# Performance work log

Hardware: AMD Instinct MI355X
Metric: run time of the kernel (lower is better)

The kernel has to match this reference:

```python
import jax, jax.numpy as jnp
import numpy as np

B, S, E, H, M, K, FF = 4, 256, 1024, 16, 65536, 32, 4096
HD = E // H
LN_EPS = 1e-5


def _ln(x, g, b):
    mu = jnp.mean(x, axis=-1, keepdims=True)
    var = jnp.var(x, axis=-1, keepdims=True)
    return (x - mu) * jax.lax.rsqrt(var + LN_EPS) * g + b


def _mha(q, k, v, wq, bq, wk, bk, wv, bv, wo, bo):
    Bq, Sq, _ = q.shape
    Sk = k.shape[1]
    Q = (q @ wq + bq).reshape(Bq, Sq, H, HD)
    Kh = (k @ wk + bk).reshape(Bq, Sk, H, HD)
    V = (v @ wv + bv).reshape(Bq, Sk, H, HD)
    scores = jnp.einsum('bqhd,bkhd->bhqk', Q, Kh) / np.float32(np.sqrt(HD))
    attn = jax.nn.softmax(scores, axis=-1)
    out = jnp.einsum('bhqk,bkhd->bqhd', attn, V).reshape(Bq, Sq, E)
    return out @ wo + bo


def setup_inputs() -> dict:
    key = jax.random.key(0)
    ks = iter(jax.random.split(key, 16))
    d = {
        'x': jax.random.normal(next(ks), (B, S, E), jnp.float32),
        'mem_keys': jax.random.normal(next(ks), (M, E), jnp.float32),
        'mem_vals': jax.random.normal(next(ks), (M, E), jnp.float32),
    }
    for p in ('sa', 'ma'):
        for w in ('wq', 'wk', 'wv', 'wo'):
            d[f'{p}_{w}'] = 0.02 * jax.random.normal(next(ks), (E, E), jnp.float32)
        for bname in ('bq', 'bk', 'bv', 'bo'):
            d[f'{p}_{bname}'] = jnp.zeros((E,), jnp.float32)
    for ln in ('ln1', 'ln2', 'ln3'):
        d[f'{ln}_g'] = jnp.ones((E,), jnp.float32)
        d[f'{ln}_b'] = jnp.zeros((E,), jnp.float32)
    d['fc1_w'] = 0.02 * jax.random.normal(next(ks), (E, FF), jnp.float32)
    d['fc1_b'] = jnp.zeros((FF,), jnp.float32)
    d['fc2_w'] = 0.02 * jax.random.normal(next(ks), (FF, E), jnp.float32)
    d['fc2_b'] = jnp.zeros((E,), jnp.float32)
    return d


def reference(x, mem_keys, mem_vals,
              sa_wq, sa_bq, sa_wk, sa_bk, sa_wv, sa_bv, sa_wo, sa_bo,
              ma_wq, ma_bq, ma_wk, ma_bk, ma_wv, ma_bv, ma_wo, ma_bo,
              ln1_g, ln1_b, ln2_g, ln2_b, ln3_g, ln3_b,
              fc1_w, fc1_b, fc2_w, fc2_b):
    # self-attention block (eval mode -> dropout is identity)
    a = _mha(x, x, x, sa_wq, sa_bq, sa_wk, sa_bk, sa_wv, sa_bv, sa_wo, sa_bo)
    x1 = _ln(x + a, ln1_g, ln1_b)
    # kNN retrieval: cosine sim -> top-k -> gather values
    qn = x1 / jnp.maximum(jnp.linalg.norm(x1, axis=-1, keepdims=True), 1e-12)
    mkn = mem_keys / jnp.maximum(jnp.linalg.norm(mem_keys, axis=-1, keepdims=True), 1e-12)
    sims = jnp.einsum('bse,me->bsm', qn, mkn)              # (B,S,M)
    _, idx = jax.lax.top_k(sims, K)                        # (B,S,K)
    retrieved = mem_vals[idx]                              # (B,S,K,E)
    rflat = retrieved.reshape(B, S * K, E)
    # memory cross-attention over retrieved values
    m = _mha(x1, rflat, rflat, ma_wq, ma_bq, ma_wk, ma_bk, ma_wv, ma_bv, ma_wo, ma_bo)
    x2 = _ln(x1 + m, ln2_g, ln2_b)
    # FFN (exact GELU, as torch default)
    h = jax.nn.gelu(x2 @ fc1_w + fc1_b, approximate=False)
    y = h @ fc2_w + fc2_b
    return _ln(x2 + y, ln3_g, ln3_b)
```

## Files before the change

kernel.cpp:

```cpp
#include <hip/hip_runtime.h>
#include <hip/hip_bf16.h>
#include <math.h>

#define DEVFN __device__ __forceinline__

typedef __attribute__((ext_vector_type(8))) short bf16x8;
typedef __attribute__((ext_vector_type(8))) unsigned short u16x8;
typedef __attribute__((ext_vector_type(4))) unsigned short u16x4;
typedef __attribute__((ext_vector_type(4))) float f32x4;

static constexpr int Bn = 4, Sn = 256, En = 1024, Hn = 16;
static constexpr int Mn = 65536, Kt = 32, FFn = 4096;
static constexpr int NT = Bn * Sn;

DEVFN unsigned short f2b(float f) {
  unsigned int u = __float_as_uint(f);
  unsigned int r = (u + 0x7FFFu + ((u >> 16) & 1u)) >> 16;
  return (unsigned short)r;
}
DEVFN float b2f(unsigned short u) { return __uint_as_float((unsigned)u << 16); }

DEVFN unsigned okey16(unsigned short u) {
  return (unsigned)(u ^ ((u >> 15) ? 0xFFFFu : 0x8000u)) & 0xFFFFu;
}

typedef const __attribute__((address_space(1))) void* as1cv_t;
typedef __attribute__((address_space(3))) void* as3v_t;
DEVFN void gload16(const void* g, void* l) {
  __builtin_amdgcn_global_load_lds((as1cv_t)g, (as3v_t)l, 16, 0, 0);
}
#define MEMFENCE asm volatile("" ::: "memory")

struct P8 { const float* s[8]; };

__global__ __launch_bounds__(256) void k_transpose8(
    P8 ps, unsigned short* __restrict__ outbase) {
  const float* in = ps.s[blockIdx.z];
  unsigned short* out = outbase + (size_t)blockIdx.z * En * En;
  __shared__ float tile[64][65];
  int tx = threadIdx.x & 63, ty = threadIdx.x >> 6;
  int c0 = blockIdx.x * 64, r0 = blockIdx.y * 64;
  #pragma unroll
  for (int i = 0; i < 16; i++) {
    int r = ty + i * 4;
    tile[tx][r] = in[(size_t)(r0 + r) * En + (c0 + tx)];
  }
  __syncthreads();
  #pragma unroll
  for (int i = 0; i < 16; i++) {
    int c = ty + i * 4;
    out[(size_t)(c0 + c) * En + (r0 + tx)] = f2b(tile[c][tx]);
  }
}

__global__ __launch_bounds__(256) void k_transpose_bf16(
    const float* __restrict__ in, unsigned short* __restrict__ out, int R, int C) {
  __shared__ float tile[64][65];
  int tx = threadIdx.x & 63, ty = threadIdx.x >> 6;
  int c0 = blockIdx.x * 64, r0 = blockIdx.y * 64;
  #pragma unroll
  for (int i = 0; i < 16; i++) {
    int r = ty + i * 4;
    tile[tx][r] = in[(size_t)(r0 + r) * C + (c0 + tx)];
  }
  __syncthreads();
  #pragma unroll
  for (int i = 0; i < 16; i++) {
    int c = ty + i * 4;
    out[(size_t)(c0 + c) * R + (r0 + tx)] = f2b(tile[c][tx]);
  }
}

__global__ __launch_bounds__(256) void k_cvt_bf16(
    const float* __restrict__ in, unsigned short* __restrict__ out, int n4) {
  int i = blockIdx.x * 256 + threadIdx.x;
  if (i >= n4) return;
  float4 v = ((const float4*)in)[i];
  uint2 o;
  o.x = (unsigned int)f2b(v.x) | ((unsigned int)f2b(v.y) << 16);
  o.y = (unsigned int)f2b(v.z) | ((unsigned int)f2b(v.w) << 16);
  ((uint2*)out)[i] = o;
}

__global__ __launch_bounds__(256) void k_gathercvt(
    const float* __restrict__ mv, const int* __restrict__ idx,
    unsigned short* __restrict__ out) {
  int r = blockIdx.x;
  int src = idx[r];
  float4 v = ((const float4*)(mv + (size_t)src * En))[threadIdx.x];
  uint2 o;
  o.x = (unsigned int)f2b(v.x) | ((unsigned int)f2b(v.y) << 16);
  o.y = (unsigned int)f2b(v.z) | ((unsigned int)f2b(v.w) << 16);
  ((uint2*)(out + (size_t)r * En))[threadIdx.x] = o;
}

__global__ __launch_bounds__(256) void k_concat3(
    const float* __restrict__ a, const float* __restrict__ b,
    const float* __restrict__ c, float* __restrict__ o) {
  int i = blockIdx.x * 256 + threadIdx.x;
  float v = (i < 1024) ? a[i] : (i < 2048) ? b[i - 1024] : c[i - 2048];
  o[i] = v;
}

__global__ __launch_bounds__(256) void k_normcvt(
    const float* __restrict__ mk, unsigned short* __restrict__ out) {
  int m = blockIdx.x, t = threadIdx.x;
  float4 v = ((const float4*)(mk + (size_t)m * En))[t];
  float ss = v.x*v.x + v.y*v.y + v.z*v.z + v.w*v.w;
  #pragma unroll
  for (int d = 32; d; d >>= 1) ss += __shfl_down(ss, d);
  __shared__ float red[4];
  int lane = t & 63, w = t >> 6;
  if (lane == 0) red[w] = ss;
  __syncthreads();
  float rs = 1.0f / fmaxf(sqrtf(red[0] + red[1] + red[2] + red[3]), 1e-12f);
  uint2 o;
  o.x = (unsigned int)f2b(v.x * rs) | ((unsigned int)f2b(v.y * rs) << 16);
  o.y = (unsigned int)f2b(v.z * rs) | ((unsigned int)f2b(v.w * rs) << 16);
  ((uint2*)(out + (size_t)m * En))[t] = o;
}

__global__ __launch_bounds__(256) void k_layernorm(
    const float* __restrict__ in, const float* __restrict__ g, const float* __restrict__ bb,
    float* __restrict__ outf, unsigned short* __restrict__ outb) {
  int n = blockIdx.x, t = threadIdx.x;
  float4 v = ((const float4*)(in + (size_t)n * En))[t];
  float s  = v.x + v.y + v.z + v.w;
  float s2 = v.x*v.x + v.y*v.y + v.z*v.z + v.w*v.w;
  #pragma unroll
  for (int d = 32; d; d >>= 1) { s += __shfl_down(s, d); s2 += __shfl_down(s2, d); }
  __shared__ float rs[4], rq[4];
  int lane = t & 63, w = t >> 6;
  if (lane == 0) { rs[w] = s; rq[w] = s2; }
  __syncthreads();
  float mean = (rs[0]+rs[1]+rs[2]+rs[3]) * (1.0f/En);
  float var  = (rq[0]+rq[1]+rq[2]+rq[3]) * (1.0f/En) - mean*mean;
  float rstd = rsqrtf(var + 1e-5f);
  float4 gg = ((const float4*)g)[t];
  float4 bv = ((const float4*)bb)[t];
  float o0 = (v.x-mean)*rstd*gg.x + bv.x;
  float o1 = (v.y-mean)*rstd*gg.y + bv.y;
  float o2 = (v.z-mean)*rstd*gg.z + bv.z;
  float o3 = (v.w-mean)*rstd*gg.w + bv.w;
  if (outf) { float4 ov = {o0,o1,o2,o3}; ((float4*)(outf + (size_t)n*En))[t] = ov; }
  if (outb) {
    uint2 o;
    o.x = (unsigned int)f2b(o0) | ((unsigned int)f2b(o1) << 16);
    o.y = (unsigned int)f2b(o2) | ((unsigned int)f2b(o3) << 16);
    ((uint2*)(outb + (size_t)n*En))[t] = o;
  }
}

__global__ __launch_bounds__(256) void k_layernorm4(
    const float* __restrict__ pp, const float* __restrict__ pbias,
    const float* __restrict__ resid,
    const float* __restrict__ g, const float* __restrict__ bb,
    float* __restrict__ outf, unsigned short* __restrict__ outb) {
  int n = blockIdx.x, t = threadIdx.x;
  const size_t PS = (size_t)NT * En / 4;
  size_t i = (size_t)n * 256 + t;
  float4 p0 = ((const float4*)pp)[i];
  float4 p1 = ((const float4*)pp)[i + PS];
  float4 p2 = ((const float4*)pp)[i + 2 * PS];
  float4 p3 = ((const float4*)pp)[i + 3 * PS];
  float4 rv = ((const float4*)(resid + (size_t)n * En))[t];
  float4 bi = ((const float4*)pbias)[t];
  float4 v;
  v.x = (p0.x + p1.x) + (p2.x + p3.x) + bi.x + rv.x;
  v.y = (p0.y + p1.y) + (p2.y + p3.y) + bi.y + rv.y;
  v.z = (p0.z + p1.z) + (p2.z + p3.z) + bi.z + rv.z;
  v.w = (p0.w + p1.w) + (p2.w + p3.w) + bi.w + rv.w;
  float s  = v.x + v.y + v.z + v.w;
  float s2 = v.x*v.x + v.y*v.y + v.z*v.z + v.w*v.w;
  #pragma unroll
  for (int d = 32; d; d >>= 1) { s += __shfl_down(s, d); s2 += __shfl_down(s2, d); }
  __shared__ float rs[4], rq[4];
  int lane = t & 63, w = t >> 6;
  if (lane == 0) { rs[w] = s; rq[w] = s2; }
  __syncthreads();
  float mean = (rs[0]+rs[1]+rs[2]+rs[3]) * (1.0f/En);
  float var  = (rq[0]+rq[1]+rq[2]+rq[3]) * (1.0f/En) - mean*mean;
  float rstd = rsqrtf(var + 1e-5f);
  float4 gg = ((const float4*)g)[t];
  float4 bv = ((const float4*)bb)[t];
  float o0 = (v.x-mean)*rstd*gg.x + bv.x;
  float o1 = (v.y-mean)*rstd*gg.y + bv.y;
  float o2 = (v.z-mean)*rstd*gg.z + bv.z;
  float o3 = (v.w-mean)*rstd*gg.w + bv.w;
  if (outf) { float4 ov = {o0,o1,o2,o3}; ((float4*)(outf + (size_t)n*En))[t] = ov; }
  if (outb) {
    uint2 o;
    o.x = (unsigned int)f2b(o0) | ((unsigned int)f2b(o1) << 16);
    o.y = (unsigned int)f2b(o2) | ((unsigned int)f2b(o3) << 16);
    ((uint2*)(outb + (size_t)n*En))[t] = o;
  }
}

template<int EPI, bool AGATHER, int NOUT, int LSWZ>
__global__ __launch_bounds__(512) void k_gemm256(
    const unsigned short* __restrict__ Ab, const unsigned short* __restrict__ Bb,
    const int* __restrict__ gidx, const float* __restrict__ bias,
    float* __restrict__ Cf, unsigned short* __restrict__ cb0, unsigned short* __restrict__ cb1,
    int Ndim, int Kdim, int nRT, int nCT) {
  extern __shared__ unsigned short lds[];
  const int t = threadIdx.x, lane = t & 63, w = t >> 6;
  const int wr = w >> 2, wc = w & 3, l15 = lane & 15, l4 = lane >> 4;
  const int lr2 = lane >> 2;
  const int cg  = (lane & 3) ^ (((lane >> 5) & 1) << 1);

  const int nwg = nRT * nCT;
  int lb = ((int)blockIdx.x % 8) * (nwg >> 3) + ((int)blockIdx.x >> 3);
  int rowT, colT;
  if (LSWZ == 0) { rowT = lb % nRT; colT = lb / nRT; }
  else           { colT = lb % nCT; rowT = lb / nCT; }
  const int row0 = rowT * 256, col0 = colT * 256;

  auto pa = [&](int h) -> unsigned short* { return lds + h * 16384; };
  auto pb = [&](int h) -> unsigned short* { return lds + h * 16384 + 8192; };

  const unsigned short *aSrc0, *aSrc1;
  if constexpr (AGATHER) {
    aSrc0 = Ab + (size_t)gidx[row0 + w * 32 + lr2] * Kdim + cg * 8;
    aSrc1 = Ab + (size_t)gidx[row0 + w * 32 + 16 + lr2] * Kdim + cg * 8;
  } else {
    aSrc0 = Ab + (size_t)(row0 + w * 32 + lr2) * Kdim + cg * 8;
    aSrc1 = aSrc0 + (size_t)16 * Kdim;
  }
  const unsigned short* bSrc0 = Bb + (size_t)(col0 + w * 32 + lr2) * Kdim + cg * 8;
  const unsigned short* bSrc1 = bSrc0 + (size_t)16 * Kdim;

  f32x4 acc[8][4];
  #pragma unroll
  for (int i = 0; i < 8; i++)
    #pragma unroll
    for (int j = 0; j < 4; j++) acc[i][j] = (f32x4){0.f, 0.f, 0.f, 0.f};

  const int NH = Kdim >> 5;
  #pragma unroll
  for (int h = 0; h < 3; ++h) {
    const int ko = h * 32;
    gload16(aSrc0 + ko, pa(h) + w*32*32);
    gload16(aSrc1 + ko, pa(h) + (w*32+16)*32);
    gload16(bSrc0 + ko, pb(h) + w*32*32);
    gload16(bSrc1 + ko, pb(h) + (w*32+16)*32);
  }
  asm volatile("s_waitcnt vmcnt(8)" ::: "memory");
  __builtin_amdgcn_s_barrier();
  MEMFENCE;

  for (int hs = 0; hs < NH; ++hs) {
    const int cur = hs & 3;
    const unsigned short* Ap = pa(cur);
    const unsigned short* Bp = pb(cur);
    const int h3 = (hs + 3) & 3, ko3 = (hs + 3) * 32;
    const bool pf = (hs + 3) < NH;
    bf16x8 bfr[4], af[4];

    #pragma unroll
    for (int ni = 0; ni < 4; ni++) {
      int row = wc * 64 + ni * 16 + l15;
      int c8 = l4 ^ (((row >> 3) & 1) << 1);
      bfr[ni] = *(const bf16x8*)&Bp[row * 32 + c8 * 8];
    }
    #pragma unroll
    for (int m = 0; m < 4; m++) {
      int row = wr * 128 + m * 16 + l15;
      int c8 = l4 ^ (((row >> 3) & 1) << 1);
      af[m] = *(const bf16x8*)&Ap[row * 32 + c8 * 8];
    }
    if (pf) {
      gload16(aSrc0 + ko3, pa(h3) + w*32*32);
      gload16(aSrc1 + ko3, pa(h3) + (w*32+16)*32);
    }
    __builtin_amdgcn_s_setprio(1);
    #pragma unroll
    for (int m = 0; m < 4; m++)
      #pragma unroll
      for (int ni = 0; ni < 4; ni++)
        acc[m][ni] = __builtin_amdgcn_mfma_f32_16x16x32_bf16(af[m], bfr[ni], acc[m][ni], 0, 0, 0);
    __builtin_amdgcn_s_setprio(0);

    #pragma unroll
    for (int m = 0; m < 4; m++) {
      int row = wr * 128 + (4 + m) * 16 + l15;
      int c8 = l4 ^ (((row >> 3) & 1) << 1);
      af[m] = *(const bf16x8*)&Ap[row * 32 + c8 * 8];
    }
    if (pf) {
      gload16(bSrc0 + ko3, pb(h3) + w*32*32);
      gload16(bSrc1 + ko3, pb(h3) + (w*32+16)*32);
    }
    __builtin_amdgcn_s_setprio(1);
    #pragma unroll
    for (int m = 0; m < 4; m++)
      #pragma unroll
      for (int ni = 0; ni < 4; ni++)
        acc[4 + m][ni] = __builtin_amdgcn_mfma_f32_16x16x32_bf16(af[m], bfr[ni], acc[4 + m][ni], 0, 0, 0);
    __builtin_amdgcn_s_setprio(0);

    if (hs + 1 < NH) {
      const int rem = NH - 2 - hs;
      if (rem >= 2)      asm volatile("s_waitcnt vmcnt(8)" ::: "memory");
      else if (rem == 1) asm volatile("s_waitcnt vmcnt(4)" ::: "memory");
      else               asm volatile("s_waitcnt vmcnt(0)" ::: "memory");
      __builtin_amdgcn_s_barrier();
      MEMFENCE;
    }
  }

  #pragma unroll
  for (int m = 0; m < 8; m++) {
    #pragma unroll
    for (int ni = 0; ni < 4; ni++) {
      int col  = col0 + wc * 64 + ni * 16 + l15;
      int rowb = row0 + wr * 128 + m * 16 + l4 * 4;
      if constexpr (EPI == 6) {
        if (col < 1024) {
          #pragma unroll
          for (int r = 0; r < 4; r++)
            cb0[(size_t)(rowb + r) * 1024 + col] = f2b(acc[m][ni][r] + bias[col]);
        } else {
          int c = col - 1024;
          int bi = rowb >> 13, k0 = rowb & 8191;
          u16x4 o;
          #pragma unroll
          for (int r = 0; r < 4; r++) o[r] = f2b(acc[m][ni][r] + bias[col]);
          *(u16x4*)&cb1[((size_t)bi * 1024 + c) * 8192 + k0] = o;
        }
      } else {
        #pragma unroll
        for (int r = 0; r < 4; r++) {
          float v = acc[m][ni][r];
          if constexpr (EPI == 4) {
            Cf[(size_t)(rowb + r) * Ndim + col] = v;
          } else if constexpr (EPI == 5) {
            cb0[(size_t)(rowb + r) * Ndim + col] = f2b(v);
          } else {
            unsigned short* cb = (col >> 10) ? cb1 : cb0;
            cb[(size_t)(rowb + r) * 1024 + (col & 1023)] = f2b(v + bias[col]);
          }
        }
      }
    }
  }
}

template<int EPI, bool AGATHER, bool SWAPG, int NOUT, bool QSC, int SK>
__global__ __launch_bounds__(256) void k_gemm(
    const unsigned short* __restrict__ Ab, const unsigned short* __restrict__ Bb,
    const int* __restrict__ gidx,
    const float* __restrict__ bias, const float* __restrict__ resid,
    float* __restrict__ Cf, unsigned short* __restrict__ cb0,
    unsigned short* __restrict__ cb1, unsigned short* __restrict__ cb2,
    int Ndim, int Kdim) {
  __shared__ unsigned short As[128][32];
  __shared__ unsigned short Bs[128][32];
  const int t = threadIdx.x, lane = t & 63, w = t >> 6;
  const int wr = w >> 1, wc = w & 1, l15 = lane & 15, l4 = lane >> 4;
  const int row0 = (SWAPG ? blockIdx.x : blockIdx.y) * 128;
  const int col0 = (SWAPG ? blockIdx.y : blockIdx.x) * 128;
  const int c8  = (lane & 3) * 8;
  const int r16 = lane >> 2;
  const int rA0 = w * 32 + r16, rA1 = rA0 + 16;
  const int koff = (SK > 1) ? (int)blockIdx.z * (Kdim / SK) : 0;
  const int kend = (SK > 1) ? koff + Kdim / SK : Kdim;

  size_t raA0, raA1, raB0, raB1;
  if constexpr (AGATHER) {
    raA0 = (size_t)gidx[row0 + rA0] * Kdim;
    raA1 = (size_t)gidx[row0 + rA1] * Kdim;
  } else {
    raA0 = (size_t)(row0 + rA0) * Kdim;
    raA1 = (size_t)(row0 + rA1) * Kdim;
  }
  raB0 = (size_t)(col0 + rA0) * Kdim;
  raB1 = (size_t)(col0 + rA1) * Kdim;

  f32x4 acc[4][4];
  #pragma unroll
  for (int i = 0; i < 4; i++)
    #pragma unroll
    for (int j = 0; j < 4; j++) acc[i][j] = (f32x4){0.f,0.f,0.f,0.f};

  for (int kt0 = koff; kt0 < kend; kt0 += 32) {
    __syncthreads();
    gload16(Ab + raA0 + kt0 + c8, &As[w * 32][0]);
    gload16(Ab + raA1 + kt0 + c8, &As[w * 32 + 16][0]);
    gload16(Bb + raB0 + kt0 + c8, &Bs[w * 32][0]);
    gload16(Bb + raB1 + kt0 + c8, &Bs[w * 32 + 16][0]);
    __syncthreads();
    bf16x8 af[4], bfr[4];
    #pragma unroll
    for (int mi = 0; mi < 4; mi++) af[mi]  = *(const bf16x8*)&As[wr*64 + mi*16 + l15][l4*8];
    #pragma unroll
    for (int ni = 0; ni < 4; ni++) bfr[ni] = *(const bf16x8*)&Bs[wc*64 + ni*16 + l15][l4*8];
    #pragma unroll
    for (int mi = 0; mi < 4; mi++)
      #pragma unroll
      for (int ni = 0; ni < 4; ni++)
        acc[mi][ni] = __builtin_amdgcn_mfma_f32_16x16x32_bf16(af[mi], bfr[ni], acc[mi][ni], 0, 0, 0);
  }

  unsigned short* cbase = cb0;
  int colsub = 0;
  float qsc = 1.0f;
  if constexpr (NOUT > 1) {
    int which = col0 >> 10;
    cbase = (which == 0) ? cb0 : (which == 1) ? cb1 : cb2;
    colsub = col0 & 1023;
    if (QSC && which == 0) qsc = 0.125f;
  } else if constexpr (QSC) {
    qsc = 0.125f;
  }
  float* Cfp = Cf;
  if constexpr (EPI == 7) Cfp = Cf + (size_t)blockIdx.z * NT * En;

  #pragma unroll
  for (int mi = 0; mi < 4; mi++) {
    #pragma unroll
    for (int ni = 0; ni < 4; ni++) {
      int col  = col0 + wc*64 + ni*16 + l15;
      int rowb = row0 + wr*64 + mi*16 + l4*4;
      #pragma unroll
      for (int r = 0; r < 4; r++) {
        float v = acc[mi][ni][r];
        size_t off = (size_t)(rowb + r) * Ndim + col;
        if constexpr (EPI == 0) {
          if constexpr (NOUT > 1) {
            int c2 = colsub + wc*64 + ni*16 + l15;
            cbase[(size_t)(rowb + r) * 1024 + c2] = f2b((v + bias[col]) * qsc);
          } else {
            cb0[off] = f2b((v + bias[col]) * qsc);
          }
        } else if constexpr (EPI == 1) {
          Cf[off] = v + bias[col] + resid[off];
        } else if constexpr (EPI == 2) {
          float u = v + bias[col];
          u = 0.5f * u * (1.0f + erff(u * 0.70710678118654752f));
          cb0[off] = f2b(u);
        } else if constexpr (EPI == 7) {
          Cfp[off] = v;
        } else {
          Cf[off] = v;
        }
      }
    }
  }
}

__global__ __launch_bounds__(256) void k_attn_sa(
    const unsigned short* __restrict__ Qp, const unsigned short* __restrict__ Kp,
    const unsigned short* __restrict__ Vp, unsigned short* __restrict__ Op, int Lk) {
  __shared__ unsigned short Ks[64][72];
  __shared__ unsigned short Vt[64][72];
  __shared__ float Ps[4][16][68];
  const int b = blockIdx.z;
  const int h = blockIdx.y, q0 = blockIdx.x * 64;
  const int t = threadIdx.x, lane = t & 63, w = t >> 6;
  const int l15 = lane & 15, l4 = lane >> 4;

  const int qrow = q0 + w * 16 + l15;
  const unsigned short* qptr = Qp + (size_t)(b * Sn + qrow) * En + h * 64 + l4 * 8;
  bf16x8 qf0 = *(const bf16x8*)qptr;
  bf16x8 qf1 = *(const bf16x8*)(qptr + 32);

  f32x4 oacc[4];
  #pragma unroll
  for (int i = 0; i < 4; i++) oacc[i] = (f32x4){0.f,0.f,0.f,0.f};
  float m_[4] = {-INFINITY, -INFINITY, -INFINITY, -INFINITY};
  float l_[4] = {0.f, 0.f, 0.f, 0.f};

  const int nkt = Lk / 64;
  for (int kt = 0; kt < nkt; ++kt) {
    __syncthreads();
    #pragma unroll
    for (int i = 0; i < 2; i++) {
      int ld = t + i * 256;
      int kr = ld >> 3, d8 = (ld & 7) * 8;
      size_t base = (size_t)(b * Lk + kt * 64 + kr) * En + h * 64 + d8;
      *(uint4*)&Ks[kr][d8] = *(const uint4*)(Kp + base);
      bf16x8 vv = *(const bf16x8*)(Vp + base);
      int colswz = kr ^ ((t & 7) << 3);
      #pragma unroll
      for (int j = 0; j < 8; j++) Vt[d8 + j][colswz] = ((unsigned short*)&vv)[j];
    }
    __syncthreads();

    f32x4 s[4];
    #pragma unroll
    for (int ni = 0; ni < 4; ni++) {
      s[ni] = (f32x4){0.f,0.f,0.f,0.f};
      bf16x8 kb0 = *(const bf16x8*)&Ks[ni*16 + l15][l4*8];
      bf16x8 kb1 = *(const bf16x8*)&Ks[ni*16 + l15][l4*8 + 32];
      s[ni] = __builtin_amdgcn_mfma_f32_16x16x32_bf16(qf0, kb0, s[ni], 0, 0, 0);
      s[ni] = __builtin_amdgcn_mfma_f32_16x16x32_bf16(qf1, kb1, s[ni], 0, 0, 0);
    }

    #pragma unroll
    for (int r = 0; r < 4; r++) {
      float mx = fmaxf(fmaxf(s[0][r], s[1][r]), fmaxf(s[2][r], s[3][r]));
      #pragma unroll
      for (int d2 = 1; d2 < 16; d2 <<= 1) mx = fmaxf(mx, __shfl_xor(mx, d2));
      float m = m_[r];
      if (mx > m + 8.f) {
        float alpha = __expf(m - mx);
        l_[r] *= alpha;
        #pragma unroll
        for (int nd = 0; nd < 4; nd++) oacc[nd][r] *= alpha;
        m = mx; m_[r] = mx;
      }
      float p0 = __expf(s[0][r] - m), p1 = __expf(s[1][r] - m);
      float p2 = __expf(s[2][r] - m), p3 = __expf(s[3][r] - m);
      s[0][r] = p0; s[1][r] = p1; s[2][r] = p2; s[3][r] = p3;
      l_[r] += (p0 + p1) + (p2 + p3);
    }

    #pragma unroll
    for (int ni = 0; ni < 4; ni++)
      #pragma unroll
      for (int r = 0; r < 4; r++)
        Ps[w][l4*4 + r][ni*16 + l15] = s[ni][r];
    asm volatile("s_waitcnt lgkmcnt(0)" ::: "memory");

    #pragma unroll
    for (int half = 0; half < 2; half++) {
      float4 pv0 = *(const float4*)&Ps[w][l15][half*32 + l4*8];
      float4 pv1 = *(const float4*)&Ps[w][l15][half*32 + l4*8 + 4];
      bf16x8 pa;
      pa[0]=(short)f2b(pv0.x); pa[1]=(short)f2b(pv0.y); pa[2]=(short)f2b(pv0.z); pa[3]=(short)f2b(pv0.w);
      pa[4]=(short)f2b(pv1.x); pa[5]=(short)f2b(pv1.y); pa[6]=(short)f2b(pv1.z); pa[7]=(short)f2b(pv1.w);
      #pragma unroll
      for (int nd = 0; nd < 4; nd++) {
        int dd = nd*16 + l15;
        bf16x8 vb = *(const bf16x8*)&Vt[dd][(half*32 + l4*8) ^ (((dd >> 3) & 7) << 3)];
        oacc[nd] = __builtin_amdgcn_mfma_f32_16x16x32_bf16(pa, vb, oacc[nd], 0, 0, 0);
      }
    }
  }

  #pragma unroll
  for (int r = 0; r < 4; r++) {
    float lv = l_[r];
    #pragma unroll
    for (int d2 = 1; d2 < 16; d2 <<= 1) lv += __shfl_xor(lv, d2);
    l_[r] = lv;
  }
  #pragma unroll
  for (int nd = 0; nd < 4; nd++)
    #pragma unroll
    for (int r = 0; r < 4; r++) {
      int q = q0 + w*16 + l4*4 + r;
      Op[(size_t)(b * Sn + q) * En + h * 64 + nd*16 + l15] = f2b(oacc[nd][r] / l_[r]);
    }
}

__global__ __launch_bounds__(256, 2) void k_attn_ma(
    const unsigned short* __restrict__ Qp, const unsigned short* __restrict__ Kp,
    const unsigned short* __restrict__ Vp,
    unsigned short* __restrict__ PO, float* __restrict__ PM, float* __restrict__ PL) {
  constexpr int Lk = Sn * Kt;
  constexpr int NTI = 8;
  __shared__ unsigned short Ks[2][64 * 64];
  __shared__ unsigned short Vt[2][64 * 64];
  __shared__ float Ps[4][16][68];
  const int sp = blockIdx.x, h = blockIdx.y, b = blockIdx.z;
  const int t = threadIdx.x, lane = t & 63, w = t >> 6;
  const int l15 = lane & 15, l4 = lane >> 4;
  const int l8 = lane >> 3, l7 = lane & 7;
  const int kswz = (l7 ^ l8) * 8;
  const int rbase = w * 16;

  bf16x8 qf[4][2];
  #pragma unroll
  for (int qt = 0; qt < 4; qt++) {
    const unsigned short* qptr = Qp + (size_t)(b * Sn + w * 64 + qt * 16 + l15) * En + h * 64 + l4 * 8;
    qf[qt][0] = *(const bf16x8*)qptr;
    qf[qt][1] = *(const bf16x8*)(qptr + 32);
  }

  f32x4 oacc[4][4];
  #pragma unroll
  for (int i = 0; i < 4; i++)
    #pragma unroll
    for (int j = 0; j < 4; j++) oacc[i][j] = (f32x4){0.f,0.f,0.f,0.f};
  float m_[4][4], l_[4][4];
  #pragma unroll
  for (int i = 0; i < 4; i++)
    #pragma unroll
    for (int j = 0; j < 4; j++) { m_[i][j] = -INFINITY; l_[i][j] = 0.f; }

  const int kt0 = sp * NTI;
  auto stage = [&](int kt, int buf) {
    #pragma unroll
    for (int i = 0; i < 2; i++) {
      int row = rbase + i * 8 + l8;
      gload16(Kp + (size_t)(b * Lk + kt * 64 + row) * En + h * 64 + kswz,
              &Ks[buf][(rbase + i * 8) * 64]);
      gload16(Vp + ((size_t)b * 1024 + h * 64 + row) * (size_t)Lk + kt * 64 + kswz,
              &Vt[buf][(rbase + i * 8) * 64]);
    }
  };

  stage(kt0, 0);
  stage(kt0 + 1, 1);
  asm volatile("s_waitcnt vmcnt(4)" ::: "memory");
  __builtin_amdgcn_s_barrier();
  MEMFENCE;

  for (int j = 0; j < NTI; ++j) {
    const int cur = j & 1;
    #pragma unroll
    for (int qt = 0; qt < 4; qt++) {
      f32x4 s[4];
      #pragma unroll
      for (int ni = 0; ni < 4; ni++) {
        s[ni] = (f32x4){0.f,0.f,0.f,0.f};
        int rowK = ni * 16 + l15, sw = (rowK & 7) * 8;
        bf16x8 kb0 = *(const bf16x8*)&Ks[cur][rowK * 64 + ((l4 * 8) ^ sw)];
        bf16x8 kb1 = *(const bf16x8*)&Ks[cur][rowK * 64 + ((l4 * 8 + 32) ^ sw)];
        s[ni] = __builtin_amdgcn_mfma_f32_16x16x32_bf16(qf[qt][0], kb0, s[ni], 0, 0, 0);
        s[ni] = __builtin_amdgcn_mfma_f32_16x16x32_bf16(qf[qt][1], kb1, s[ni], 0, 0, 0);
      }
      #pragma unroll
      for (int r = 0; r < 4; r++) {
        float mx = fmaxf(fmaxf(s[0][r], s[1][r]), fmaxf(s[2][r], s[3][r]));
        #pragma unroll
        for (int d2 = 1; d2 < 16; d2 <<= 1) mx = fmaxf(mx, __shfl_xor(mx, d2));
        float m = m_[qt][r];
        if (mx > m + 8.f) {
          float alpha = __expf(m - mx);
          l_[qt][r] *= alpha;
          #pragma unroll
          for (int nd = 0; nd < 4; nd++) oacc[qt][nd][r] *= alpha;
          m = mx; m_[qt][r] = mx;
        }
        float p0 = __expf(s[0][r] - m), p1 = __expf(s[1][r] - m);
        float p2 = __expf(s[2][r] - m), p3 = __expf(s[3][r] - m);
        s[0][r] = p0; s[1][r] = p1; s[2][r] = p2; s[3][r] = p3;
        l_[qt][r] += (p0 + p1) + (p2 + p3);
      }
      #pragma unroll
      for (int ni = 0; ni < 4; ni++)
        #pragma unroll
        for (int r = 0; r < 4; r++)
          Ps[w][l4*4 + r][ni*16 + l15] = s[ni][r];
      asm volatile("s_waitcnt lgkmcnt(0)" ::: "memory");
      #pragma unroll
      for (int half = 0; half < 2; half++) {
        float4 pv0 = *(const float4*)&Ps[w][l15][half*32 + l4*8];
        float4 pv1 = *(const float4*)&Ps[w][l15][half*32 + l4*8 + 4];
        bf16x8 pa;
        pa[0]=(short)f2b(pv0.x); pa[1]=(short)f2b(pv0.y); pa[2]=(short)f2b(pv0.z); pa[3]=(short)f2b(pv0.w);
        pa[4]=(short)f2b(pv1.x); pa[5]=(short)f2b(pv1.y); pa[6]=(short)f2b(pv1.z); pa[7]=(short)f2b(pv1.w);
        #pragma unroll
        for (int nd = 0; nd < 4; nd++) {
          int dd = nd*16 + l15;
          bf16x8 vb = *(const bf16x8*)&Vt[cur][dd * 64 + ((half*32 + l4*8) ^ ((dd & 7) * 8))];
          oacc[qt][nd] = __builtin_amdgcn_mfma_f32_16x16x32_bf16(pa, vb, oacc[qt][nd], 0, 0, 0);
        }
      }
    }
    MEMFENCE; __builtin_amdgcn_s_barrier(); MEMFENCE;
    if (j + 2 < NTI) stage(kt0 + j + 2, cur);
    if (j + 1 < NTI) {
      if (j + 2 < NTI) asm volatile("s_waitcnt vmcnt(4)" ::: "memory");
      else             asm volatile("s_waitcnt vmcnt(0)" ::: "memory");
      __builtin_amdgcn_s_barrier();
      MEMFENCE;
    }
  }

  #pragma unroll
  for (int qt = 0; qt < 4; qt++)
    #pragma unroll
    for (int r = 0; r < 4; r++) {
      float lv = l_[qt][r];
      #pragma unroll
      for (int d2 = 1; d2 < 16; d2 <<= 1) lv += __shfl_xor(lv, d2);
      l_[qt][r] = lv;
    }

  const int slot = (b * Hn + h) * 16 + sp;
  #pragma unroll
  for (int qt = 0; qt < 4; qt++)
    #pragma unroll
    for (int nd = 0; nd < 4; nd++)
      #pragma unroll
      for (int r = 0; r < 4; r++)
        PO[(size_t)slot * 16384 + (w*64 + qt*16 + l4*4 + r) * 64 + nd*16 + l15] = f2b(oacc[qt][nd][r]);
  if (l15 == 0) {
    #pragma unroll
    for (int qt = 0; qt < 4; qt++)
      #pragma unroll
      for (int r = 0; r < 4; r++) {
        PM[slot * 256 + w*64 + qt*16 + l4*4 + r] = m_[qt][r];
        PL[slot * 256 + w*64 + qt*16 + l4*4 + r] = l_[qt][r];
      }
  }
}

__global__ __launch_bounds__(256) void k_attn_comb16(
    const unsigned short* __restrict__ PO, const float* __restrict__ PM,
    const float* __restrict__ PL, unsigned short* __restrict__ Op) {
  const int W = blockIdx.x * 4 + (threadIdx.x >> 6);
  const int lane = threadIdx.x & 63;
  const int bh = W >> 8, q = W & 255;
  const int slotBase = bh * 16;
  float ms[16];
  float M = -INFINITY;
  #pragma unroll
  for (int s = 0; s < 16; s++) { ms[s] = PM[(slotBase + s) * 256 + q]; M = fmaxf(M, ms[s]); }
  float L = 0.f, acc = 0.f;
  #pragma unroll
  for (int s = 0; s < 16; s++) {
    float wgt = __expf(ms[s] - M);
    L += PL[(slotBase + s) * 256 + q] * wgt;
    acc += wgt * b2f(PO[(size_t)(slotBase + s) * 16384 + q * 64 + lane]);
  }
  const int b = bh >> 4, h = bh & 15;
  Op[(size_t)(b * Sn + q) * En + h * 64 + lane] = f2b(acc / L);
}

DEVFN unsigned blk_exscan16(unsigned part, volatile unsigned* wsum, int lane, int wid) {
  unsigned v = part;
  #pragma unroll
  for (int d = 1; d < 64; d <<= 1) { unsigned o = __shfl_up(v, d); if (lane >= d) v += o; }
  if (lane == 63) wsum[wid] = v;
  __syncthreads();
  unsigned woff = 0;
  for (int i = 0; i < wid; i++) woff += wsum[i];
  unsigned r = woff + v - part;
  __syncthreads();
  return r;
}

DEVFN void find_thr16(const unsigned* hist, int NB, unsigned need,
                      int t, int lane, int wid, volatile unsigned* wsum,
                      volatile int* s_thr, volatile unsigned* s_above) {
  int per = NB >> 10;
  int lo = NB - per * (t + 1);
  unsigned part = 0;
  for (int j = 0; j < per; j++) part += hist[lo + j];
  unsigned ex = blk_exscan16(part, wsum, lane, wid);
  if (ex < need && ex + part >= need) {
    unsigned c = ex;
    for (int j = per - 1; j >= 0; j--) {
      unsigned h = hist[lo + j];
      if (c + h >= need) { *s_thr = lo + j; *s_above = c; break; }
      c += h;
    }
  }
  __syncthreads();
}

__global__ __launch_bounds__(1024) void k_topk16(
    const unsigned short* __restrict__ simsb, int* __restrict__ oidx) {
  const int n = blockIdx.x, t = threadIdx.x;
  const int lane = t & 63, wid = t >> 6;
  const u16x8* row8 = (const u16x8*)(simsb + (size_t)n * Mn);
  constexpr unsigned CAP = 2048;
  __shared__ unsigned hist[2048];
  __shared__ unsigned wsum[16];
  __shared__ int s_thr;
  __shared__ unsigned s_above;
  __shared__ unsigned h2[32];
  __shared__ unsigned s_cnt, s_na;
  __shared__ unsigned short ckey[CAP];
  __shared__ unsigned cidx[CAP];
  __shared__ int slist[32];
  __shared__ unsigned sL, sneedEq, scntEq, s_imin;

  for (int i = t; i < 2048; i += 1024) hist[i] = 0;
  if (t < 32) h2[t] = 0;
  if (t == 0) { s_cnt = 0; s_na = 0; }
  __syncthreads();

  {
    u16x8 v = row8[3584 + t];
    #pragma unroll
    for (int j = 0; j < 8; j++) atomicAdd(&hist[okey16(v[j]) >> 5], 1u);
  }
  __syncthreads();
  find_thr16(hist, 2048, 32, t, lane, wid, wsum, &s_thr, &s_above);
  const unsigned base = ((unsigned)s_thr) << 5;

  #pragma unroll
  for (int p = 0; p < 8; p++) {
    u16x8 v = row8[p * 1024 + t];
    unsigned i0 = (unsigned)(p * 1024 + t) * 8;
    #pragma unroll
    for (int j = 0; j < 8; j++) {
      unsigned k = okey16(v[j]);
      if (k >= base) {
        unsigned slot = atomicAdd(&s_cnt, 1u);
        if (slot < CAP) { ckey[slot] = (unsigned short)k; cidx[slot] = i0 + j; }
      }
    }
  }
// ... 117 lines not shown
    unsigned cnt = 0;
    for (int p = 0; p < 8; p++) {
      u16x8 v = row8[p * 1024 + t];
      unsigned i0 = (unsigned)(p * 1024 + t) * 8;
      #pragma unroll
      for (int j = 0; j < 8; j++) {
        unsigned k = okey16(v[j]);
        cnt += (k > L || (k == L && i0 + j <= istar));
      }
    }
    unsigned pos = blk_exscan16(cnt, wsum, lane, wid);
    for (int p = 0; p < 8; p++) {
      u16x8 v = row8[p * 1024 + t];
      unsigned i0 = (unsigned)(p * 1024 + t) * 8;
      #pragma unroll
      for (int j = 0; j < 8; j++) {
        unsigned k = okey16(v[j]);
        if (k > L || (k == L && i0 + j <= istar)) oidx[n * Kt + pos++] = (int)(i0 + j);
      }
    }
  }
}

extern "C" void kernel_launch(void* const* d_in, const int* in_sizes, int n_in,
                              void* d_out, int out_size, void* d_ws, size_t ws_size,
                              hipStream_t stream) {
  (void)in_sizes; (void)n_in; (void)out_size;
  const float* x      = (const float*)d_in[0];
  const float* mem_k  = (const float*)d_in[1];
  const float* mem_v  = (const float*)d_in[2];
  const float* sa_w[4] = {(const float*)d_in[3], (const float*)d_in[4], (const float*)d_in[5], (const float*)d_in[6]};
  const float* sa_b[4] = {(const float*)d_in[7], (const float*)d_in[8], (const float*)d_in[9], (const float*)d_in[10]};
  const float* ma_w[4] = {(const float*)d_in[11], (const float*)d_in[12], (const float*)d_in[13], (const float*)d_in[14]};
  const float* ma_b[4] = {(const float*)d_in[15], (const float*)d_in[16], (const float*)d_in[17], (const float*)d_in[18]};
  const float* ln_g[3] = {(const float*)d_in[19], (const float*)d_in[21], (const float*)d_in[23]};
  const float* ln_b[3] = {(const float*)d_in[20], (const float*)d_in[22], (const float*)d_in[24]};
  const float* fc1_w = (const float*)d_in[25];
  const float* fc1_b = (const float*)d_in[26];
  const float* fc2_w = (const float*)d_in[27];
  const float* fc2_b = (const float*)d_in[28];
  float* out = (float*)d_out;

  char* ws = (char*)d_ws;
  size_t off = 0;
  auto alloc = [&](size_t bytes) -> char* {
    char* p = ws + off;
    off = (off + bytes + 255) & ~(size_t)255;
    return p;
  };

  unsigned short* wt[8];
  for (int i = 0; i < 8; i++) wt[i] = (unsigned short*)alloc((size_t)En * En * 2);
  unsigned short* fc1t  = (unsigned short*)alloc((size_t)FFn * En * 2);
  unsigned short* fc2t  = (unsigned short*)alloc((size_t)En * FFn * 2);
  unsigned short* xb    = (unsigned short*)alloc((size_t)NT * En * 2);
  unsigned short* Qb    = (unsigned short*)alloc((size_t)NT * En * 2);
  unsigned short* Kb    = (unsigned short*)alloc((size_t)NT * En * 2);
  unsigned short* Vb    = (unsigned short*)alloc((size_t)NT * En * 2);
  unsigned short* at1b  = (unsigned short*)alloc((size_t)NT * En * 2);
  float*          x1f   = (float*)alloc((size_t)NT * En * 4);
  unsigned short* x1b   = (unsigned short*)alloc((size_t)NT * En * 2);
  char*           simsRaw = alloc((size_t)NT * Mn * 4);
  int*            idx   = (int*)alloc((size_t)NT * Kt * 4);
  unsigned short* K2b   = (unsigned short*)alloc((size_t)NT * Kt * En * 2);
  unsigned short* V2b   = (unsigned short*)alloc((size_t)NT * Kt * En * 2);
  unsigned short* Q2b   = (unsigned short*)alloc((size_t)NT * En * 2);
  unsigned short* at2b  = (unsigned short*)alloc((size_t)NT * En * 2);
  float*          x2f   = (float*)alloc((size_t)NT * En * 4);
  unsigned short* x2b   = (unsigned short*)alloc((size_t)NT * En * 2);
  unsigned short* hb    = (unsigned short*)alloc((size_t)NT * FFn * 2);
  float*          pp    = (float*)alloc((size_t)4 * NT * En * 4);
  float*          bcat_sa = (float*)alloc(3072 * 4);
  float*          bcat_ma = (float*)alloc(2048 * 4);

  if (off > ws_size) return;

  unsigned short* simsb = (unsigned short*)simsRaw;
  unsigned short* mkb = (unsigned short*)K2b;
  unsigned short* Ab2 = (unsigned short*)(simsRaw + (size_t)128 * 1024 * 1024);
  unsigned short* PO  = (unsigned short*)(simsRaw + (size_t)192 * 1024 * 1024);
  float* PM = (float*)(simsRaw + (size_t)224 * 1024 * 1024);
  float* PL = (float*)(simsRaw + (size_t)225 * 1024 * 1024);

  (void)hipFuncSetAttribute((const void*)&k_gemm256<5,false,1,0>,
                            hipFuncAttributeMaxDynamicSharedMemorySize, 131072);
  (void)hipFuncSetAttribute((const void*)&k_gemm256<6,false,2,1>,
                            hipFuncAttributeMaxDynamicSharedMemorySize, 131072);

  P8 p8;
  for (int i = 0; i < 4; i++) { p8.s[i] = sa_w[i]; p8.s[4 + i] = ma_w[i]; }
  k_transpose8<<<dim3(16, 16, 8), 256, 0, stream>>>(p8, wt[0]);
  k_transpose_bf16<<<dim3(64, 16), 256, 0, stream>>>(fc1_w, fc1t, En, FFn);
  k_transpose_bf16<<<dim3(16, 64), 256, 0, stream>>>(fc2_w, fc2t, FFn, En);
  k_concat3<<<dim3(12), 256, 0, stream>>>(sa_b[0], sa_b[1], sa_b[2], bcat_sa);
  k_concat3<<<dim3(8),  256, 0, stream>>>(ma_b[1], ma_b[2], ma_b[2], bcat_ma);

  k_cvt_bf16<<<dim3(NT * En / 4 / 256), 256, 0, stream>>>(x, xb, NT * En / 4);
  k_normcvt<<<dim3(Mn), 256, 0, stream>>>(mem_k, mkb);

  const dim3 g1(En / 128, NT / 128);
  const dim3 g1s(En / 128, NT / 128, 4);

  k_gemm<0,false,false,3,true,1><<<dim3(24, 8), 256, 0, stream>>>(xb, wt[0], nullptr, bcat_sa, nullptr, nullptr, Qb, Kb, Vb, 3072, En);
  k_attn_sa<<<dim3(Sn / 64, Hn, Bn), 256, 0, stream>>>(Qb, Kb, Vb, at1b, Sn);
  k_gemm<7,false,false,1,false,4><<<g1s, 256, 0, stream>>>(at1b, wt[3], nullptr, nullptr, nullptr, pp, nullptr, nullptr, nullptr, En, En);
  k_layernorm4<<<NT, 256, 0, stream>>>(pp, sa_b[3], x, ln_g[0], ln_b[0], x1f, x1b);

  k_gemm256<5,false,1,0><<<dim3(1024), 512, 131072, stream>>>(
      x1b, mkb, nullptr, nullptr, nullptr, simsb, nullptr, Mn, En, NT / 256, Mn / 256);
  k_topk16<<<NT, 1024, 0, stream>>>(simsb, idx);

  k_gathercvt<<<dim3(NT * Kt), 256, 0, stream>>>(mem_v, idx, Ab2);
  k_gemm256<6,false,2,1><<<dim3(1024), 512, 131072, stream>>>(
      Ab2, wt[5], nullptr, bcat_ma, nullptr, K2b, V2b, 2048, En, NT * Kt / 256, 2048 / 256);
  k_gemm<0,false,false,1,true,1><<<g1, 256, 0, stream>>>(x1b, wt[4], nullptr, ma_b[0], nullptr, nullptr, Q2b, nullptr, nullptr, En, En);
  k_attn_ma<<<dim3(16, Hn, Bn), 256, 0, stream>>>(Q2b, K2b, V2b, PO, PM, PL);
  k_attn_comb16<<<dim3(Bn * Hn * Sn / 4), 256, 0, stream>>>(PO, PM, PL, at2b);
  k_gemm<7,false,false,1,false,4><<<g1s, 256, 0, stream>>>(at2b, wt[7], nullptr, nullptr, nullptr, pp, nullptr, nullptr, nullptr, En, En);
  k_layernorm4<<<NT, 256, 0, stream>>>(pp, ma_b[3], x1f, ln_g[1], ln_b[1], x2f, x2b);

  k_gemm<2,false,false,1,false,1><<<dim3(FFn / 128, NT / 128), 256, 0, stream>>>(x2b, fc1t, nullptr, fc1_b, nullptr, nullptr, hb, nullptr, nullptr, FFn, En);
  k_gemm<7,false,false,1,false,4><<<g1s, 256, 0, stream>>>(hb, fc2t, nullptr, nullptr, nullptr, pp, nullptr, nullptr, nullptr, En, FFn);
  k_layernorm4<<<NT, 256, 0, stream>>>(pp, fc2_b, x2f, ln_g[2], ln_b[2], out, nullptr);
}
```

Measured before the change: 791.1 us.

## Triple-buffer k_gemm K-loop with async LDS loads and fold log2e into Q scale

The 128x128 k_gemm loses its two-barrier single-buffer loop. It now uses a 3-stage LDS ring filled by global_load_lds with XOR-swizzled columns, waits on vmcnt so loads overlap the MFMAs, and raises wave priority around the MFMA block. The Q scale is changed from 1/sqrt(d) to 1/sqrt(d)*log2(e) so the attention softmax kernels can use exp2f instead of __expf. Unused gather, residual-epilogue and layernorm paths are removed. LDS use per block triples, which may lower occupancy.

```diff
diff --git a/kernel.cpp b/kernel.cpp
--- a/kernel.cpp
+++ b/kernel.cpp
@@ -12,6 +12,7 @@
 static constexpr int Bn = 4, Sn = 256, En = 1024, Hn = 16;
 static constexpr int Mn = 65536, Kt = 32, FFn = 4096;
 static constexpr int NT = Bn * Sn;
+static constexpr float QS = 0.18033688011112042f;
 
 DEVFN unsigned short f2b(float f) {
   unsigned int u = __float_as_uint(f);
@@ -118,37 +119,6 @@
   o.x = (unsigned int)f2b(v.x * rs) | ((unsigned int)f2b(v.y * rs) << 16);
   o.y = (unsigned int)f2b(v.z * rs) | ((unsigned int)f2b(v.w * rs) << 16);
   ((uint2*)(out + (size_t)m * En))[t] = o;
-}
-
-__global__ __launch_bounds__(256) void k_layernorm(
-    const float* __restrict__ in, const float* __restrict__ g, const float* __restrict__ bb,
-    float* __restrict__ outf, unsigned short* __restrict__ outb) {
-  int n = blockIdx.x, t = threadIdx.x;
-  float4 v = ((const float4*)(in + (size_t)n * En))[t];
-  float s  = v.x + v.y + v.z + v.w;
-  float s2 = v.x*v.x + v.y*v.y + v.z*v.z + v.w*v.w;
-  #pragma unroll
-  for (int d = 32; d; d >>= 1) { s += __shfl_down(s, d); s2 += __shfl_down(s2, d); }
-  __shared__ float rs[4], rq[4];
-  int lane = t & 63, w = t >> 6;
-  if (lane == 0) { rs[w] = s; rq[w] = s2; }
-  __syncthreads();
-  float mean = (rs[0]+rs[1]+rs[2]+rs[3]) * (1.0f/En);
-  float var  = (rq[0]+rq[1]+rq[2]+rq[3]) * (1.0f/En) - mean*mean;
-  float rstd = rsqrtf(var + 1e-5f);
-  float4 gg = ((const float4*)g)[t];
-  float4 bv = ((const float4*)bb)[t];
-  float o0 = (v.x-mean)*rstd*gg.x + bv.x;
-  float o1 = (v.y-mean)*rstd*gg.y + bv.y;
-  float o2 = (v.z-mean)*rstd*gg.z + bv.z;
-  float o3 = (v.w-mean)*rstd*gg.w + bv.w;
-  if (outf) { float4 ov = {o0,o1,o2,o3}; ((float4*)(outf + (size_t)n*En))[t] = ov; }
-  if (outb) {
-    uint2 o;
-    o.x = (unsigned int)f2b(o0) | ((unsigned int)f2b(o1) << 16);
-    o.y = (unsigned int)f2b(o2) | ((unsigned int)f2b(o3) << 16);
-    ((uint2*)(outb + (size_t)n*En))[t] = o;
-  }
 }
 
 __global__ __launch_bounds__(256) void k_layernorm4(
@@ -196,10 +166,10 @@
   }
 }
 
-template<int EPI, bool AGATHER, int NOUT, int LSWZ>
+template<int EPI, int NOUT, int LSWZ>
 __global__ __launch_bounds__(512) void k_gemm256(
     const unsigned short* __restrict__ Ab, const unsigned short* __restrict__ Bb,
-    const int* __restrict__ gidx, const float* __restrict__ bias,
+    const float* __restrict__ bias,
     float* __restrict__ Cf, unsigned short* __restrict__ cb0, unsigned short* __restrict__ cb1,
     int Ndim, int Kdim, int nRT, int nCT) {
   extern __shared__ unsigned short lds[];
@@ -218,14 +188,8 @@
   auto pa = [&](int h) -> unsigned short* { return lds + h * 16384; };
   auto pb = [&](int h) -> unsigned short* { return lds + h * 16384 + 8192; };
 
-  const unsigned short *aSrc0, *aSrc1;
-  if constexpr (AGATHER) {
-    aSrc0 = Ab + (size_t)gidx[row0 + w * 32 + lr2] * Kdim + cg * 8;
-    aSrc1 = Ab + (size_t)gidx[row0 + w * 32 + 16 + lr2] * Kdim + cg * 8;
-  } else {
-    aSrc0 = Ab + (size_t)(row0 + w * 32 + lr2) * Kdim + cg * 8;
-    aSrc1 = aSrc0 + (size_t)16 * Kdim;
-  }
+  const unsigned short* aSrc0 = Ab + (size_t)(row0 + w * 32 + lr2) * Kdim + cg * 8;
+  const unsigned short* aSrc1 = aSrc0 + (size_t)16 * Kdim;
   const unsigned short* bSrc0 = Bb + (size_t)(col0 + w * 32 + lr2) * Kdim + cg * 8;
   const unsigned short* bSrc1 = bSrc0 + (size_t)16 * Kdim;
 
@@ -329,52 +293,34 @@
         }
       } else {
         #pragma unroll
-        for (int r = 0; r < 4; r++) {
-          float v = acc[m][ni][r];
-          if constexpr (EPI == 4) {
-            Cf[(size_t)(rowb + r) * Ndim + col] = v;
-          } else if constexpr (EPI == 5) {
-            cb0[(size_t)(rowb + r) * Ndim + col] = f2b(v);
-          } else {
-            unsigned short* cb = (col >> 10) ? cb1 : cb0;
-            cb[(size_t)(rowb + r) * 1024 + (col & 1023)] = f2b(v + bias[col]);
-          }
-        }
-      }
-    }
-  }
-}
-
-template<int EPI, bool AGATHER, bool SWAPG, int NOUT, bool QSC, int SK>
+        for (int r = 0; r < 4; r++)
+          cb0[(size_t)(rowb + r) * Ndim + col] = f2b(acc[m][ni][r]);
+      }
+    }
+  }
+}
+
+template<int EPI, int NOUT, bool QSC, int SK>
 __global__ __launch_bounds__(256) void k_gemm(
     const unsigned short* __restrict__ Ab, const unsigned short* __restrict__ Bb,
-    const int* __restrict__ gidx,
-    const float* __restrict__ bias, const float* __restrict__ resid,
+    const float* __restrict__ bias,
     float* __restrict__ Cf, unsigned short* __restrict__ cb0,
     unsigned short* __restrict__ cb1, unsigned short* __restrict__ cb2,
     int Ndim, int Kdim) {
-  __shared__ unsigned short As[128][32];
-  __shared__ unsigned short Bs[128][32];
+  __shared__ unsigned short ring[3][2][128 * 32];
   const int t = threadIdx.x, lane = t & 63, w = t >> 6;
   const int wr = w >> 1, wc = w & 1, l15 = lane & 15, l4 = lane >> 4;
-  const int row0 = (SWAPG ? blockIdx.x : blockIdx.y) * 128;
-  const int col0 = (SWAPG ? blockIdx.y : blockIdx.x) * 128;
-  const int c8  = (lane & 3) * 8;
-  const int r16 = lane >> 2;
-  const int rA0 = w * 32 + r16, rA1 = rA0 + 16;
+  const int lr2 = lane >> 2;
+  const int cg  = (lane & 3) ^ (((lane >> 5) & 1) << 1);
+  const int row0 = blockIdx.y * 128;
+  const int col0 = blockIdx.x * 128;
   const int koff = (SK > 1) ? (int)blockIdx.z * (Kdim / SK) : 0;
-  const int kend = (SK > 1) ? koff + Kdim / SK : Kdim;
-
-  size_t raA0, raA1, raB0, raB1;
-  if constexpr (AGATHER) {
-    raA0 = (size_t)gidx[row0 + rA0] * Kdim;
-    raA1 = (size_t)gidx[row0 + rA1] * Kdim;
-  } else {
-    raA0 = (size_t)(row0 + rA0) * Kdim;
-    raA1 = (size_t)(row0 + rA1) * Kdim;
-  }
-  raB0 = (size_t)(col0 + rA0) * Kdim;
-  raB1 = (size_t)(col0 + rA1) * Kdim;
+  const int NH = ((SK > 1) ? (Kdim / SK) : Kdim) >> 5;
+
+  const unsigned short* aSrc0 = Ab + (size_t)(row0 + w * 32 + lr2) * Kdim + koff + cg * 8;
+  const unsigned short* aSrc1 = aSrc0 + (size_t)16 * Kdim;
+  const unsigned short* bSrc0 = Bb + (size_t)(col0 + w * 32 + lr2) * Kdim + koff + cg * 8;
+  const unsigned short* bSrc1 = bSrc0 + (size_t)16 * Kdim;
 
   f32x4 acc[4][4];
   #pragma unroll
@@ -382,23 +328,55 @@
     #pragma unroll
     for (int j = 0; j < 4; j++) acc[i][j] = (f32x4){0.f,0.f,0.f,0.f};
 
-  for (int kt0 = koff; kt0 < kend; kt0 += 32) {
-    __syncthreads();
-    gload16(Ab + raA0 + kt0 + c8, &As[w * 32][0]);
-    gload16(Ab + raA1 + kt0 + c8, &As[w * 32 + 16][0]);
-    gload16(Bb + raB0 + kt0 + c8, &Bs[w * 32][0]);
-    gload16(Bb + raB1 + kt0 + c8, &Bs[w * 32 + 16][0]);
-    __syncthreads();
+  auto stage = [&](int h, int buf) {
+    const int ko = h * 32;
+    gload16(aSrc0 + ko, &ring[buf][0][w * 32 * 32]);
+    gload16(aSrc1 + ko, &ring[buf][0][(w * 32 + 16) * 32]);
+    gload16(bSrc0 + ko, &ring[buf][1][w * 32 * 32]);
+    gload16(bSrc1 + ko, &ring[buf][1][(w * 32 + 16) * 32]);
+  };
+
+  stage(0, 0);
+  stage(1, 1);
+  asm volatile("s_waitcnt vmcnt(4)" ::: "memory");
+  __builtin_amdgcn_s_barrier();
+  MEMFENCE;
+
+  int cur = 0;
+  for (int hs = 0; hs < NH; ++hs) {
+    const unsigned short* Ap = &ring[cur][0][0];
+    const unsigned short* Bp = &ring[cur][1][0];
     bf16x8 af[4], bfr[4];
     #pragma unroll
-    for (int mi = 0; mi < 4; mi++) af[mi]  = *(const bf16x8*)&As[wr*64 + mi*16 + l15][l4*8];
-    #pragma unroll
-    for (int ni = 0; ni < 4; ni++) bfr[ni] = *(const bf16x8*)&Bs[wc*64 + ni*16 + l15][l4*8];
+    for (int ni = 0; ni < 4; ni++) {
+      int row = wc * 64 + ni * 16 + l15;
+      int c8 = l4 ^ (((row >> 3) & 1) << 1);
+      bfr[ni] = *(const bf16x8*)&Bp[row * 32 + c8 * 8];
+    }
+    #pragma unroll
+    for (int m = 0; m < 4; m++) {
+      int row = wr * 64 + m * 16 + l15;
+      int c8 = l4 ^ (((row >> 3) & 1) << 1);
+      af[m] = *(const bf16x8*)&Ap[row * 32 + c8 * 8];
+    }
+    if (hs + 2 < NH) {
+      int nb = cur + 2; if (nb >= 3) nb -= 3;
+      stage(hs + 2, nb);
+    }
+    __builtin_amdgcn_s_setprio(1);
     #pragma unroll
     for (int mi = 0; mi < 4; mi++)
       #pragma unroll
       for (int ni = 0; ni < 4; ni++)
         acc[mi][ni] = __builtin_amdgcn_mfma_f32_16x16x32_bf16(af[mi], bfr[ni], acc[mi][ni], 0, 0, 0);
+    __builtin_amdgcn_s_setprio(0);
+    if (hs + 1 < NH) {
+      if (hs + 2 < NH) asm volatile("s_waitcnt vmcnt(4)" ::: "memory");
+      else             asm volatile("s_waitcnt vmcnt(0)" ::: "memory");
+      __builtin_amdgcn_s_barrier();
+      MEMFENCE;
+    }
+    cur = cur + 1; if (cur >= 3) cur -= 3;
   }
 
   unsigned short* cbase = cb0;
@@ -408,9 +386,9 @@
     int which = col0 >> 10;
     cbase = (which == 0) ? cb0 : (which == 1) ? cb1 : cb2;
     colsub = col0 & 1023;
-    if (QSC && which == 0) qsc = 0.125f;
+    if (QSC && which == 0) qsc = QS;
   } else if constexpr (QSC) {
-    qsc = 0.125f;
+    qsc = QS;
   }
   float* Cfp = Cf;
   if constexpr (EPI == 7) Cfp = Cf + (size_t)blockIdx.z * NT * En;
@@ -432,8 +410,6 @@
           } else {
             cb0[off] = f2b((v + bias[col]) * qsc);
           }
-        } else if constexpr (EPI == 1) {
-          Cf[off] = v + bias[col] + resid[off];
         } else if constexpr (EPI == 2) {
           float u = v + bias[col];
           u = 0.5f * u * (1.0f + erff(u * 0.70710678118654752f));
@@ -503,14 +479,14 @@
       for (int d2 = 1; d2 < 16; d2 <<= 1) mx = fmaxf(mx, __shfl_xor(mx, d2));
       float m = m_[r];
       if (mx > m + 8.f) {
-        float alpha = __expf(m - mx);
+        float alpha = exp2f(m - mx);
         l_[r] *= alpha;
         #pragma unroll
         for (int nd = 0; nd < 4; nd++) oacc[nd][r] *= alpha;
         m = mx; m_[r] = mx;
       }
-      float p0 = __expf(s[0][r] - m), p1 = __expf(s[1][r] - m);
-      float p2 = __expf(s[2][r] - m), p3 = __expf(s[3][r] - m);
+      float p0 = exp2f(s[0][r] - m), p1 = exp2f(s[1][r] - m);
+      float p2 = exp2f(s[2][r] - m), p3 = exp2f(s[3][r] - m);
       s[0][r] = p0; s[1][r] = p1; s[2][r] = p2; s[3][r] = p3;
       l_[r] += (p0 + p1) + (p2 + p3);
     }
@@ -628,14 +604,14 @@
         for (int d2 = 1; d2 < 16; d2 <<= 1) mx = fmaxf(mx, __shfl_xor(mx, d2));
         float m = m_[qt][r];
         if (mx > m + 8.f) {
-          float alpha = __expf(m - mx);
+          float alpha = exp2f(m - mx);
           l_[qt][r] *= alpha;
           #pragma unroll
           for (int nd = 0; nd < 4; nd++) oacc[qt][nd][r] *= alpha;
           m = mx; m_[qt][r] = mx;
         }
-        float p0 = __expf(s[0][r] - m), p1 = __expf(s[1][r] - m);
-        float p2 = __expf(s[2][r] - m), p3 = __expf(s[3][r] - m);
+        float p0 = exp2f(s[0][r] - m), p1 = exp2f(s[1][r] - m);
+        float p2 = exp2f(s[2][r] - m), p3 = exp2f(s[3][r] - m);
         s[0][r] = p0; s[1][r] = p1; s[2][r] = p2; s[3][r] = p3;
         l_[qt][r] += (p0 + p1) + (p2 + p3);
       }
@@ -713,7 +689,7 @@
   float L = 0.f, acc = 0.f;
   #pragma unroll
   for (int s = 0; s < 16; s++) {
-    float wgt = __expf(ms[s] - M);
+    float wgt = exp2f(ms[s] - M);
     L += PL[(slotBase + s) * 256 + q] * wgt;
     acc += wgt * b2f(PO[(size_t)(slotBase + s) * 16384 + q * 64 + lane]);
   }
@@ -997,9 +973,9 @@
   float* PM = (float*)(simsRaw + (size_t)224 * 1024 * 1024);
   float* PL = (float*)(simsRaw + (size_t)225 * 1024 * 1024);
 
-  (void)hipFuncSetAttribute((const void*)&k_gemm256<5,false,1,0>,
+  (void)hipFuncSetAttribute((const void*)&k_gemm256<5,1,0>,
                             hipFuncAttributeMaxDynamicSharedMemorySize, 131072);
-  (void)hipFuncSetAttribute((const void*)&k_gemm256<6,false,2,1>,
+  (void)hipFuncSetAttribute((const void*)&k_gemm256<6,2,1>,
                             hipFuncAttributeMaxDynamicSharedMemorySize, 131072);
 
   P8 p8;
@@ -1016,25 +992,25 @@
   const dim3 g1(En / 128, NT / 128);
   const dim3 g1s(En / 128, NT / 128, 4);
 
-  k_gemm<0,false,false,3,true,1><<<dim3(24, 8), 256, 0, stream>>>(xb, wt[0], nullptr, bcat_sa, nullptr, nullptr, Qb, Kb, Vb, 3072, En);
+  k_gemm<0,3,true,1><<<dim3(24, 8), 256, 0, stream>>>(xb, wt[0], bcat_sa, nullptr, Qb, Kb, Vb, 3072, En);
   k_attn_sa<<<dim3(Sn / 64, Hn, Bn), 256, 0, stream>>>(Qb, Kb, Vb, at1b, Sn);
-  k_gemm<7,false,false,1,false,4><<<g1s, 256, 0, stream>>>(at1b, wt[3], nullptr, nullptr, nullptr, pp, nullptr, nullptr, nullptr, En, En);
+  k_gemm<7,1,false,4><<<g1s, 256, 0, stream>>>(at1b, wt[3], nullptr, pp, nullptr, nullptr, nullptr, En, En);
   k_layernorm4<<<NT, 256, 0, stream>>>(pp, sa_b[3], x, ln_g[0], ln_b[0], x1f, x1b);
 
-  k_gemm256<5,false,1,0><<<dim3(1024), 512, 131072, stream>>>(
-      x1b, mkb, nullptr, nullptr, nullptr, simsb, nullptr, Mn, En, NT / 256, Mn / 256);
+  k_gemm256<5,1,0><<<dim3(1024), 512, 131072, stream>>>(
+      x1b, mkb, nullptr, nullptr, simsb, nullptr, Mn, En, NT / 256, Mn / 256);
   k_topk16<<<NT, 1024, 0, stream>>>(simsb, idx);
 
   k_gathercvt<<<dim3(NT * Kt), 256, 0, stream>>>(mem_v, idx, Ab2);
-  k_gemm256<6,false,2,1><<<dim3(1024), 512, 131072, stream>>>(
-      Ab2, wt[5], nullptr, bcat_ma, nullptr, K2b, V2b, 2048, En, NT * Kt / 256, 2048 / 256);
-  k_gemm<0,false,false,1,true,1><<<g1, 256, 0, stream>>>(x1b, wt[4], nullptr, ma_b[0], nullptr, nullptr, Q2b, nullptr, nullptr, En, En);
+  k_gemm256<6,2,1><<<dim3(1024), 512, 131072, stream>>>(
+      Ab2, wt[5], bcat_ma, nullptr, K2b, V2b, 2048, En, NT * Kt / 256, 2048 / 256);
+  k_gemm<0,1,true,1><<<g1, 256, 0, stream>>>(x1b, wt[4], ma_b[0], nullptr, Q2b, nullptr, nullptr, En, En);
   k_attn_ma<<<dim3(16, Hn, Bn), 256, 0, stream>>>(Q2b, K2b, V2b, PO, PM, PL);
   k_attn_comb16<<<dim3(Bn * Hn * Sn / 4), 256, 0, stream>>>(PO, PM, PL, at2b);
-  k_gemm<7,false,false,1,false,4><<<g1s, 256, 0, stream>>>(at2b, wt[7], nullptr, nullptr, nullptr, pp, nullptr, nullptr, nullptr, En, En);
+  k_gemm<7,1,false,4><<<g1s, 256, 0, stream>>>(at2b, wt[7], nullptr, pp, nullptr, nullptr, nullptr, En, En);
   k_layernorm4<<<NT, 256, 0, stream>>>(pp, ma_b[3], x1f, ln_g[1], ln_b[1], x2f, x2b);
 
-  k_gemm<2,false,false,1,false,1><<<dim3(FFn / 128, NT / 128), 256, 0, stream>>>(x2b, fc1t, nullptr, fc1_b, nullptr, nullptr, hb, nullptr, nullptr, FFn, En);
-  k_gemm<7,false,false,1,false,4><<<g1s, 256, 0, stream>>>(hb, fc2t, nullptr, nullptr, nullptr, pp, nullptr, nullptr, nullptr, En, FFn);
+  k_gemm<2,1,false,1><<<dim3(FFn / 128, NT / 128), 256, 0, stream>>>(x2b, fc1t, fc1_b, nullptr, hb, nullptr, nullptr, FFn, En);
+  k_gemm<7,1,false,4><<<g1s, 256, 0, stream>>>(hb, fc2t, nullptr, pp, nullptr, nullptr, nullptr, En, FFn);
   k_layernorm4<<<NT, 256, 0, stream>>>(pp, fc2_b, x2f, ln_g[2], ln_b[2], out, nullptr);
 }
```

After: 749.5 us. -5.2%, faster.
